# Optimization experiments

Hardware: AMD Instinct MI355X
Metric: run time of the kernel (lower is better)

Reference implementation:

```python
import jax, jax.numpy as jnp
import numpy as np

# static config (mirrors init_kwargs)
F_T, S = 8, 24            # video_shape = (F_T, S, S)
K, DIL = 3, 1             # kernel_size, dilation (same for all 3 axes)
HEADS, DHEAD, DIM = 8, 64, 512
INNER = HEADS * DHEAD
PAD = DIL * (K - 1)       # causal: pad 2 at the FRONT of each spatial axis
KJ = K ** 3               # 27 neighbors per query
N_VID = F_T * S * S       # 4608 video tokens


def causal_pad(t):
    # t: [B, D, F, S, S] -> pad front of f/h/w axes (torch F.pad (PAD*?,0) causal layout)
    return jnp.pad(t, ((0, 0), (0, 0), (PAD, 0), (PAD, 0), (PAD, 0)))


def unfold3d(t):
    # torch unfoldNd equivalent. t: [B, D, F+PAD, S+PAD, S+PAD]
    # returns [B, N_VID, KJ, D]; kernel offsets ordered (kf, kh, kw) w fastest,
    # matching torch unfold's channel-major / kernel-minor layout after the
    # rearrange 'b (d j) i -> b i j d'.
    sl = []
    for i in range(K):
        for j in range(K):
            for kk in range(K):
                sl.append(t[:, :, i * DIL:i * DIL + F_T,
                                  j * DIL:j * DIL + S,
                                  kk * DIL:kk * DIL + S])
    u = jnp.stack(sl, axis=2)                      # [B, D, KJ, F, S, S]
    B, D = t.shape[0], t.shape[1]
    u = u.reshape(B, D, KJ, N_VID)
    return jnp.transpose(u, (0, 3, 2, 1))          # [B, N_VID, KJ, D]


def make_mask():
    # True where the neighbor falls into zero padding (out-of-range / future under causal pad)
    ones = jnp.ones((1, 1, F_T, S, S), jnp.float32)
    u = unfold3d(causal_pad(ones))[0, :, :, 0]     # [N_VID, KJ]
    m = u == 0.0
    return jnp.pad(m, ((0, 0), (1, 0)), constant_values=False)  # bos col never masked


def stable_softmax(t, alpha=32.0 ** 2):
    t = t / alpha
    t = t - jax.lax.stop_gradient(jnp.max(t, axis=-1, keepdims=True))
    return jax.nn.softmax(t * alpha, axis=-1)


def setup_inputs() -> dict:
    key = jax.random.key(0)
    ks = jax.random.split(key, 9)
    return {
        "x": jax.random.normal(ks[0], (1, N_VID + 1, DIM), jnp.float32),
        "Wq": jax.random.normal(ks[1], (DIM, INNER), jnp.float32) * 0.02,
        "Wkv": jax.random.normal(ks[2], (DIM, 2 * INNER), jnp.float32) * 0.02,
        "W_th": jax.random.normal(ks[3], (HEADS, HEADS), jnp.float32) * 0.2,
        "Wout": jax.random.normal(ks[4], (INNER, DIM), jnp.float32) * 0.02,
        "bout": jax.random.normal(ks[5], (DIM,), jnp.float32) * 0.02,
        "ax1": jax.random.normal(ks[6], (K, HEADS), jnp.float32),
        "ax2": jax.random.normal(ks[7], (K, HEADS), jnp.float32),
        "ax3": jax.random.normal(ks[8], (K, HEADS), jnp.float32),
    }


def reference(x, Wq, Wkv, W_th, Wout, bout, ax1, ax2, ax3):
    b, n, _ = x.shape                       # b=1, n = 1 + N_VID (no extra padding)
    h, d = HEADS, DHEAD
    scale = d ** -0.5

    q = x @ Wq
    k, v = jnp.split(x @ Wkv, 2, axis=-1)

    def to_heads(t):  # 'b n (h d) -> (b h) n d'
        return t.reshape(b, n, h, d).transpose(0, 2, 1, 3).reshape(b * h, n, d)

    q, k, v = map(to_heads, (q, k, v))
    q = q[:, 1:] * scale                    # drop bos query
    k_bos, v_bos = k[:, :1], v[:, :1]       # [bh, 1, d]
    k, v = k[:, 1:], v[:, 1:]

    def to_vid(t):  # 'b (f h w) d -> b d f h w'
        return t.reshape(b * h, F_T, S, S, d).transpose(0, 4, 1, 2, 3)

    ku = unfold3d(causal_pad(to_vid(k)))    # [bh, N, KJ, d]
    vu = unfold3d(causal_pad(to_vid(v)))
    N = ku.shape[1]

    kb = jnp.broadcast_to(k_bos[:, :, None, :], (b * h, N, 1, d))
    vb = jnp.broadcast_to(v_bos[:, :, None, :], (b * h, N, 1, d))
    ku = jnp.concatenate([kb, ku], axis=2)  # [bh, N, KJ+1, d]
    vu = jnp.concatenate([vb, vu], axis=2)

    sim = jnp.einsum('bid,bijd->bij', q, ku)                 # [bh, N, KJ+1]

    # axial relative position bias over the 3x3x3 kernel, pad 0 for bos column
    rel = (ax1[:, None, None, :] + ax2[None, :, None, :] + ax3[None, None, :, :])
    rel = rel.reshape(KJ, h)                                 # [27, h]
    bias = jnp.pad(rel.T[:, None, :], ((0, 0), (0, 0), (1, 0)))  # [h, 1, KJ+1]

    sim = sim.reshape(b, h, N, KJ + 1) + bias[None]
    mask = make_mask()                                       # [N, KJ+1]
    sim = jnp.where(mask[None, None], -jnp.finfo(sim.dtype).max, sim)

    attn = stable_softmax(sim)                               # [b, h, N, KJ+1]
    attn = jnp.einsum('hg,bgij->bhij', W_th, attn)           # talking heads 1x1 conv

    out = jnp.einsum('bhij,bhijd->bhid', attn, vu.reshape(b, h, N, KJ + 1, d))
    out = jnp.concatenate([v_bos.reshape(b, h, 1, d), out], axis=2)  # re-attach bos value
    out = out.transpose(0, 2, 1, 3).reshape(b, n, h * d)     # '(b h) n d -> b n (h d)'
    return out @ Wout + bout
```

## Files before the change

### kernel.cpp

```cpp
#include <hip/hip_runtime.h>
#include <hip/hip_bf16.h>


constexpr int TFR   = 8;
constexpr int SDIM  = 24;
constexpr int NVID  = TFR * SDIM * SDIM;
constexpr int NTOK  = NVID + 1;
constexpr int NH    = 8;
constexpr int DM    = 512;
constexpr int NJ    = 28;

typedef __attribute__((ext_vector_type(8))) short bf16x8;
typedef __attribute__((ext_vector_type(8))) unsigned short ushort8;
typedef __attribute__((ext_vector_type(4))) float f32x4;

__device__ __forceinline__ float bf2f(unsigned short u) {
    return __uint_as_float((unsigned)u << 16);
}
__device__ __forceinline__ unsigned short f2bf(float f) {
    __hip_bfloat16 h = __float2bfloat16(f);
    return reinterpret_cast<unsigned short&>(h);
}

constexpr int CAST_BLOCKS = (NTOK * DM / 4 + 255) / 256;

__global__ __launch_bounds__(256)
void prep_kernel(const float* __restrict__ x,
                 const float* __restrict__ Wq, const float* __restrict__ Wkv,
                 const float* __restrict__ Wout,
                 __hip_bfloat16* __restrict__ Xb,
                 __hip_bfloat16* __restrict__ Wqkvt,
                 __hip_bfloat16* __restrict__ Woutt)
{
    const int b   = blockIdx.x;
    const int tid = threadIdx.x;

    if (b < CAST_BLOCKS) {
        const int i = (b * 256 + tid) * 4;
        if (i >= NTOK * DM) return;
        const float4 v = *(const float4*)(x + i);
        Xb[i + 0] = __float2bfloat16(v.x);
        Xb[i + 1] = __float2bfloat16(v.y);
        Xb[i + 2] = __float2bfloat16(v.z);
        Xb[i + 3] = __float2bfloat16(v.w);
        return;
    }

    __shared__ float t[32][33];
    int tb = b - CAST_BLOCKS;
    const float* W; __hip_bfloat16* Wt; int Nd, tX, rowOff;
    if (tb < 256)      { W = Wq;   Wt = Wqkvt; Nd = 512;  tX = 16; rowOff = 0;   }
    else if (tb < 768) { tb -= 256; W = Wkv;  Wt = Wqkvt; Nd = 1024; tX = 32; rowOff = 512; }
    else               { tb -= 768; W = Wout; Wt = Woutt; Nd = 512;  tX = 16; rowOff = 0;   }
    const int n0 = (tb % tX) * 32, k0 = (tb / tX) * 32;
    const int r  = tid >> 3;
    const int c4 = (tid & 7) * 4;
    const float4 v = *(const float4*)(W + (size_t)(k0 + r) * Nd + n0 + c4);
    t[r][c4 + 0] = v.x; t[r][c4 + 1] = v.y; t[r][c4 + 2] = v.z; t[r][c4 + 3] = v.w;
    __syncthreads();
    #pragma unroll
    for (int j = 0; j < 4; ++j)
        Wt[(size_t)(rowOff + n0 + r) * 512 + k0 + c4 + j] = __float2bfloat16(t[c4 + j][r]);
}

template<int MODE>
__global__ __launch_bounds__(256)
void gemm_bt(const __hip_bfloat16* __restrict__ A,
             const __hip_bfloat16* __restrict__ Bt,
             float* __restrict__ C, __hip_bfloat16* __restrict__ Cb,
             int M, int N, int K, const float* __restrict__ bias)
{
    constexpr int BM = 64, BN = 64, BK = 64, PITCH = 72;
    __shared__ short As[BM * PITCH];
    __shared__ short Bs[BN * PITCH];

    const int tid  = threadIdx.x;
    const int m0   = blockIdx.x * BM;
    const int n0   = blockIdx.y * BN;
    const int lane = tid & 63;
    const int wave = tid >> 6;
    const int wm   = (wave >> 1) * 32;
    const int wn   = (wave & 1) * 32;
    const int col  = lane & 15;
    const int quad = lane >> 4;

    f32x4 acc[2][2] = {};

    for (int k0 = 0; k0 < K; k0 += BK) {
        #pragma unroll
        for (int it = 0; it < 2; ++it) {
            const int idx = tid + it * 256;
            const int r = idx >> 3, c = idx & 7;
            const int gr = m0 + r;
            int4 val = make_int4(0, 0, 0, 0);
            if (gr < M)
                val = *(const int4*)(A + (size_t)gr * K + k0 + c * 8);
            *(int4*)(&As[r * PITCH + c * 8]) = val;
        }
        #pragma unroll
        for (int it = 0; it < 2; ++it) {
            const int idx = tid + it * 256;
            const int r = idx >> 3, c = idx & 7;
            const int4 val = *(const int4*)(Bt + (size_t)(n0 + r) * K + k0 + c * 8);
            *(int4*)(&Bs[r * PITCH + c * 8]) = val;
        }
        __syncthreads();

        #pragma unroll
        for (int ks = 0; ks < 2; ++ks) {
            bf16x8 af[2], bfr[2];
            #pragma unroll
            for (int mt = 0; mt < 2; ++mt)
                af[mt] = *(const bf16x8*)(&As[(wm + mt * 16 + col) * PITCH + ks * 32 + quad * 8]);
            #pragma unroll
            for (int nt = 0; nt < 2; ++nt)
                bfr[nt] = *(const bf16x8*)(&Bs[(wn + nt * 16 + col) * PITCH + ks * 32 + quad * 8]);
            #pragma unroll
            for (int mt = 0; mt < 2; ++mt)
                #pragma unroll
                for (int nt = 0; nt < 2; ++nt)
                    acc[mt][nt] = __builtin_amdgcn_mfma_f32_16x16x32_bf16(
                        af[mt], bfr[nt], acc[mt][nt], 0, 0, 0);
        }
        __syncthreads();
    }

    #pragma unroll
    for (int mt = 0; mt < 2; ++mt) {
        #pragma unroll
        for (int r = 0; r < 4; ++r) {
            const int row = m0 + wm + mt * 16 + quad * 4 + r;
            if (row >= M) continue;
            #pragma unroll
            for (int nt = 0; nt < 2; ++nt) {
                const int cg = n0 + wn + nt * 16 + col;
                float v = acc[mt][nt][r];
                if (MODE == 0) {
                    if (bias) v += bias[cg];
                    C[(size_t)row * N + cg] = v;
                } else {
                    if (cg < 512) C[(size_t)row * 512 + cg] = v;
                    else          Cb[(size_t)row * 1024 + (cg - 512)] = __float2bfloat16(v);
                }
            }
        }
    }
}

__global__ __launch_bounds__(256)
void attn_v2(const float* __restrict__ Q, const __hip_bfloat16* __restrict__ KVb,
             __hip_bfloat16* __restrict__ O,
             const float* __restrict__ W_th,
             const float* __restrict__ ax1, const float* __restrict__ ax2,
             const float* __restrict__ ax3)
{
    __shared__ float attn_s[4][NH * NJ];
    __shared__ float mixed_s[4][NH * NJ];

    const int tid  = threadIdx.x;
    const int wave = tid >> 6;
    const int lane = tid & 63;
    const int g    = lane >> 3;
    const int s    = lane & 7;
    const int i    = __builtin_amdgcn_readfirstlane(blockIdx.x * 4 + (tid >> 6));
    const int qrow = i + 1;

    const int t  = i / (SDIM * SDIM);
    const int rm = i % (SDIM * SDIM);
    const int y  = rm / SDIM;
    const int x  = rm % SDIM;

    float qf[8];
    {
        const float4 q0 = *(const float4*)(Q + (size_t)qrow * DM + lane * 8);
        const float4 q1 = *(const float4*)(Q + (size_t)qrow * DM + lane * 8 + 4);
        qf[0] = q0.x * 0.125f; qf[1] = q0.y * 0.125f; qf[2] = q0.z * 0.125f; qf[3] = q0.w * 0.125f;
        qf[4] = q1.x * 0.125f; qf[5] = q1.y * 0.125f; qf[6] = q1.z * 0.125f; qf[7] = q1.w * 0.125f;
    }
    float a1[3], a2[3], a3[3];
    #pragma unroll
    for (int d = 0; d < 3; ++d) {
        a1[d] = ax1[d * NH + g];
        a2[d] = ax2[d * NH + g];
        a3[d] = ax3[d * NH + g];
    }

    float sim[NJ];
    #pragma unroll
    for (int j = 0; j < NJ; ++j) {
        int row; bool valid; float bias;
        if (j == 0) { row = 0; valid = true; bias = 0.f; }
        else {
            const int jp = j - 1;
            const int di = jp / 9, dj = (jp / 3) % 3, dk = jp % 3;
            const int tt = t + di - 2, yy = y + dj - 2, xx = x + dk - 2;
            valid = (tt >= 0) && (yy >= 0) && (xx >= 0);
            row = 1 + tt * SDIM * SDIM + yy * SDIM + xx;
            bias = a1[di] + a2[dj] + a3[dk];
        }
        if (valid) {
            const ushort8 kv = *(const ushort8*)(KVb + (size_t)row * 1024 + lane * 8);
            float p = 0.f;
            #pragma unroll
            for (int e = 0; e < 8; ++e) p += bf2f(kv[e]) * qf[e];
            p += __shfl_xor(p, 1);
            p += __shfl_xor(p, 2);
            p += __shfl_xor(p, 4);
            sim[j] = p + bias;
        } else {
            sim[j] = -1e30f;
        }
    }

    float m = -1e30f;
    #pragma unroll
    for (int j = 0; j < NJ; ++j) m = fmaxf(m, sim[j]);
    float ssum = 0.f;
    #pragma unroll
    for (int j = 0; j < NJ; ++j) { sim[j] = __expf(sim[j] - m); ssum += sim[j]; }
    const float inv = 1.f / ssum;
    #pragma unroll
    for (int j = 0; j < NJ; ++j) sim[j] *= inv;

    if (s == 0) {
        #pragma unroll
        for (int u = 0; u < 7; ++u) {
            f32x4 v4 = { sim[4*u], sim[4*u+1], sim[4*u+2], sim[4*u+3] };
            *(f32x4*)(&attn_s[wave][g * NJ + 4 * u]) = v4;
        }
    }
    __syncthreads();

    if (tid < NH * NJ) {
        const int h = tid / NJ, j = tid % NJ;
        #pragma unroll
        for (int q = 0; q < 4; ++q) {
            float acc = 0.f;
            #pragma unroll
            for (int gg = 0; gg < NH; ++gg)
                acc += W_th[h * NH + gg] * attn_s[q][gg * NJ + j];
            mixed_s[q][h * NJ + j] = acc;
        }
    }
    __syncthreads();

    float acc8[8] = {};
    #pragma unroll
    for (int j = 0; j < NJ; ++j) {
        int row; bool valid;
        if (j == 0) { row = 0; valid = true; }
        else {
            const int jp = j - 1;
            const int di = jp / 9, dj = (jp / 3) % 3, dk = jp % 3;
            const int tt = t + di - 2, yy = y + dj - 2, xx = x + dk - 2;
            valid = (tt >= 0) && (yy >= 0) && (xx >= 0);
            row = 1 + tt * SDIM * SDIM + yy * SDIM + xx;
        }
        if (valid) {
            const ushort8 vv = *(const ushort8*)(KVb + (size_t)row * 1024 + 512 + lane * 8);
            const float w = mixed_s[wave][g * NJ + j];
            #pragma unroll
            for (int e = 0; e < 8; ++e) acc8[e] += w * bf2f(vv[e]);
        }
    }

    ushort8 o;
    #pragma unroll
    for (int e = 0; e < 8; ++e) o[e] = f2bf(acc8[e]);
    *(ushort8*)(O + (size_t)qrow * DM + lane * 8) = o;

    if (i == 0) {
        const ushort8 vb = *(const ushort8*)(KVb + 512 + lane * 8);
        *(ushort8*)(O + lane * 8) = vb;
    }
}

extern "C" void kernel_launch(void* const* d_in, const int* in_sizes, int n_in,
                              void* d_out, int out_size, void* d_ws, size_t ws_size,
                              hipStream_t stream)
{
    const float* x    = (const float*)d_in[0];
    const float* Wq   = (const float*)d_in[1];
    const float* Wkv  = (const float*)d_in[2];
    const float* W_th = (const float*)d_in[3];
    const float* Wout = (const float*)d_in[4];
    const float* bout = (const float*)d_in[5];
    const float* ax1  = (const float*)d_in[6];
    const float* ax2  = (const float*)d_in[7];
    const float* ax3  = (const float*)d_in[8];
    float* out = (float*)d_out;

    char* p = (char*)d_ws;
    float* Qf = (float*)p;                         p += (size_t)NTOK * DM * 4;
    __hip_bfloat16* KVb   = (__hip_bfloat16*)p;    p += (size_t)NTOK * 2 * DM * 2;
    __hip_bfloat16* Xb    = (__hip_bfloat16*)p;    p += (size_t)NTOK * DM * 2;
    __hip_bfloat16* Ob    = (__hip_bfloat16*)p;    p += (size_t)NTOK * DM * 2;
    __hip_bfloat16* Wqkvt = (__hip_bfloat16*)p;    p += (size_t)3 * DM * DM * 2;
    __hip_bfloat16* Woutt = (__hip_bfloat16*)p;    p += (size_t)DM * DM * 2;

    const dim3 blk(256);
    const int mtiles = (NTOK + 63) / 64;

    prep_kernel<<<CAST_BLOCKS + 1024, blk, 0, stream>>>(x, Wq, Wkv, Wout, Xb, Wqkvt, Woutt);

    gemm_bt<1><<<dim3(mtiles, 24), blk, 0, stream>>>(Xb, Wqkvt, Qf, KVb,
                                                     NTOK, 3 * DM, DM, nullptr);

    attn_v2<<<dim3(NVID / 4), blk, 0, stream>>>(Qf, KVb, Ob, W_th, ax1, ax2, ax3);

    gemm_bt<0><<<dim3(mtiles, 8), blk, 0, stream>>>(Ob, Woutt, out, nullptr,
                                                    NTOK, DM, DM, bout);
}
```

Baseline: 141.6 us.

## Enlarge GEMM tiles and load tiles directly into XOR-swizzled LDS

Replaces the fixed 64x64 GEMM with a templated MFMA GEMM using 128x128 tiles for the QKV projection and 128x64 tiles for the output projection. Each wave now computes up to 4x4 MFMA tiles. Tiles are loaded with global_load_lds straight into LDS, using an XOR swizzle instead of padded rows to avoid bank conflicts. The aim is more data reuse per block and fewer register round-trips on loads. In exchange it drops the row bounds guard, so the last M tile reads past the input into adjacent workspace; those rows are discarded.

```diff
diff --git a/kernel.cpp b/kernel.cpp
--- a/kernel.cpp
+++ b/kernel.cpp
@@ -14,12 +14,11 @@
 typedef __attribute__((ext_vector_type(8))) unsigned short ushort8;
 typedef __attribute__((ext_vector_type(4))) float f32x4;
 
+typedef const __attribute__((address_space(1))) unsigned int* gas_ptr;
+typedef __attribute__((address_space(3))) unsigned int* las_ptr;
+
 __device__ __forceinline__ float bf2f(unsigned short u) {
     return __uint_as_float((unsigned)u << 16);
-}
-__device__ __forceinline__ unsigned short f2bf(float f) {
-    __hip_bfloat16 h = __float2bfloat16(f);
-    return reinterpret_cast<unsigned short&>(h);
 }
 
 constexpr int CAST_BLOCKS = (NTOK * DM / 4 + 255) / 256;
@@ -63,84 +62,93 @@
         Wt[(size_t)(rowOff + n0 + r) * 512 + k0 + c4 + j] = __float2bfloat16(t[c4 + j][r]);
 }
 
-template<int MODE>
+template<int BM, int BN, int AM, int AN, int MODE>
 __global__ __launch_bounds__(256)
-void gemm_bt(const __hip_bfloat16* __restrict__ A,
-             const __hip_bfloat16* __restrict__ Bt,
-             float* __restrict__ C, __hip_bfloat16* __restrict__ Cb,
-             int M, int N, int K, const float* __restrict__ bias)
+void gemm_mfma(const __hip_bfloat16* __restrict__ A,
+               const __hip_bfloat16* __restrict__ Bt,
+               float* __restrict__ C, __hip_bfloat16* __restrict__ Cb,
+               int M, int N, int K, const float* __restrict__ bias)
 {
-    constexpr int BM = 64, BN = 64, BK = 64, PITCH = 72;
-    __shared__ short As[BM * PITCH];
-    __shared__ short Bs[BN * PITCH];
+    constexpr int BK = 64;
+    __shared__ __align__(16) short As[BM * BK];
+    __shared__ __align__(16) short Bs[BN * BK];
 
     const int tid  = threadIdx.x;
     const int m0   = blockIdx.x * BM;
     const int n0   = blockIdx.y * BN;
     const int lane = tid & 63;
     const int wave = tid >> 6;
-    const int wm   = (wave >> 1) * 32;
-    const int wn   = (wave & 1) * 32;
+    const int wm   = (wave >> 1) * (AM * 16);
+    const int wn   = (wave & 1) * (AN * 16);
     const int col  = lane & 15;
     const int quad = lane >> 4;
 
-    f32x4 acc[2][2] = {};
+    f32x4 acc[AM][AN] = {};
 
     for (int k0 = 0; k0 < K; k0 += BK) {
         #pragma unroll
-        for (int it = 0; it < 2; ++it) {
-            const int idx = tid + it * 256;
-            const int r = idx >> 3, c = idx & 7;
-            const int gr = m0 + r;
-            int4 val = make_int4(0, 0, 0, 0);
-            if (gr < M)
-                val = *(const int4*)(A + (size_t)gr * K + k0 + c * 8);
-            *(int4*)(&As[r * PITCH + c * 8]) = val;
-        }
-        #pragma unroll
-        for (int it = 0; it < 2; ++it) {
-            const int idx = tid + it * 256;
-            const int r = idx >> 3, c = idx & 7;
-            const int4 val = *(const int4*)(Bt + (size_t)(n0 + r) * K + k0 + c * 8);
-            *(int4*)(&Bs[r * PITCH + c * 8]) = val;
+        for (int it = 0; it < BM * 8 / 256; ++it) {
+            const int idx = it * 256 + tid;
+            const int r   = idx >> 3;
+            const int u   = (idx & 7) ^ (r & 7);
+            const __hip_bfloat16* gp = A + (size_t)(m0 + r) * K + k0 + u * 8;
+            __builtin_amdgcn_global_load_lds(
+                (gas_ptr)gp, (las_ptr)&As[(it * 256 + wave * 64) * 8], 16, 0, 0);
+        }
+        #pragma unroll
+        for (int it = 0; it < BN * 8 / 256; ++it) {
+            const int idx = it * 256 + tid;
+            const int r   = idx >> 3;
+            const int u   = (idx & 7) ^ (r & 7);
+            const __hip_bfloat16* gp = Bt + (size_t)(n0 + r) * K + k0 + u * 8;
+            __builtin_amdgcn_global_load_lds(
+                (gas_ptr)gp, (las_ptr)&Bs[(it * 256 + wave * 64) * 8], 16, 0, 0);
         }
         __syncthreads();
 
         #pragma unroll
         for (int ks = 0; ks < 2; ++ks) {
-            bf16x8 af[2], bfr[2];
-            #pragma unroll
-            for (int mt = 0; mt < 2; ++mt)
-                af[mt] = *(const bf16x8*)(&As[(wm + mt * 16 + col) * PITCH + ks * 32 + quad * 8]);
-            #pragma unroll
-            for (int nt = 0; nt < 2; ++nt)
-                bfr[nt] = *(const bf16x8*)(&Bs[(wn + nt * 16 + col) * PITCH + ks * 32 + quad * 8]);
-            #pragma unroll
-            for (int mt = 0; mt < 2; ++mt)
+            bf16x8 af[AM], bfr[AN];
+            #pragma unroll
+            for (int mt = 0; mt < AM; ++mt) {
+                const int r = wm + mt * 16 + col;
+                const int u = (ks * 4 + quad) ^ (r & 7);
+                af[mt] = *(const bf16x8*)(&As[r * BK + u * 8]);
+            }
+            #pragma unroll
+            for (int nt = 0; nt < AN; ++nt) {
+                const int r = wn + nt * 16 + col;
+                const int u = (ks * 4 + quad) ^ (r & 7);
+                bfr[nt] = *(const bf16x8*)(&Bs[r * BK + u * 8]);
+            }
+            #pragma unroll
+            for (int mt = 0; mt < AM; ++mt)
                 #pragma unroll
-                for (int nt = 0; nt < 2; ++nt)
+                for (int nt = 0; nt < AN; ++nt)
                     acc[mt][nt] = __builtin_amdgcn_mfma_f32_16x16x32_bf16(
                         af[mt], bfr[nt], acc[mt][nt], 0, 0, 0);
         }
         __syncthreads();
     }
 
-    #pragma unroll
-    for (int mt = 0; mt < 2; ++mt) {
+    const bool isQ = (MODE == 1) && (n0 < 512);
+    #pragma unroll
+    for (int mt = 0; mt < AM; ++mt) {
         #pragma unroll
         for (int r = 0; r < 4; ++r) {
             const int row = m0 + wm + mt * 16 + quad * 4 + r;
             if (row >= M) continue;
             #pragma unroll
-            for (int nt = 0; nt < 2; ++nt) {
+            for (int nt = 0; nt < AN; ++nt) {
                 const int cg = n0 + wn + nt * 16 + col;
                 float v = acc[mt][nt][r];
                 if (MODE == 0) {
                     if (bias) v += bias[cg];
                     C[(size_t)row * N + cg] = v;
+                } else if (isQ) {
+                    C[(size_t)row * 512 + cg] = v;
                 } else {
-                    if (cg < 512) C[(size_t)row * 512 + cg] = v;
-                    else          Cb[(size_t)row * 1024 + (cg - 512)] = __float2bfloat16(v);
+                    Cb[(size_t)row * 1024 + (cg - 512)] = __float2bfloat16(v);
                 }
             }
         }
@@ -264,10 +272,10 @@
         }
     }
 
-    ushort8 o;
-    #pragma unroll
-    for (int e = 0; e < 8; ++e) o[e] = f2bf(acc8[e]);
-    *(ushort8*)(O + (size_t)qrow * DM + lane * 8) = o;
+    __hip_bfloat16 o[8];
+    #pragma unroll
+    for (int e = 0; e < 8; ++e) o[e] = __float2bfloat16(acc8[e]);
+    *(ushort8*)(O + (size_t)qrow * DM + lane * 8) = *(const ushort8*)o;
 
     if (i == 0) {
         const ushort8 vb = *(const ushort8*)(KVb + 512 + lane * 8);
@@ -299,15 +307,15 @@
     __hip_bfloat16* Woutt = (__hip_bfloat16*)p;    p += (size_t)DM * DM * 2;
 
     const dim3 blk(256);
-    const int mtiles = (NTOK + 63) / 64;
+    const int mtiles = (NTOK + 127) / 128;
 
     prep_kernel<<<CAST_BLOCKS + 1024, blk, 0, stream>>>(x, Wq, Wkv, Wout, Xb, Wqkvt, Woutt);
 
-    gemm_bt<1><<<dim3(mtiles, 24), blk, 0, stream>>>(Xb, Wqkvt, Qf, KVb,
-                                                     NTOK, 3 * DM, DM, nullptr);
+    gemm_mfma<128, 128, 4, 4, 1><<<dim3(mtiles, 12), blk, 0, stream>>>(
+        Xb, Wqkvt, Qf, KVb, NTOK, 3 * DM, DM, nullptr);
 
     attn_v2<<<dim3(NVID / 4), blk, 0, stream>>>(Qf, KVb, Ob, W_th, ax1, ax2, ax3);
 
-    gemm_bt<0><<<dim3(mtiles, 8), blk, 0, stream>>>(Ob, Woutt, out, nullptr,
-                                                    NTOK, DM, DM, bout);
-}
+    gemm_mfma<128, 64, 4, 2, 0><<<dim3(mtiles, 8), blk, 0, stream>>>(
+        Ob, Woutt, out, nullptr, NTOK, DM, DM, bout);
+}
```

After: 140.2 us. No clear change (-1.0%).

## Fuse fp32-to-bf16 casts into GEMM loads and enlarge GEMM tiles

Applied to the files above, without the earlier changes.

Drops the separate prep kernel that cast x and transposed the weights to bf16. Both GEMMs now read fp32 A and untransposed fp32 B directly and convert to bf16 while staging into shared memory. Tiles grow from 64x64 to 128x128, the Q 1/8 scale moves into the GEMM epilogue, and the attention output becomes fp32. This saves a launch and the bf16 intermediates, but doubles global read bytes for the operands, adds transpose-scatter stores to LDS, and cuts the grid to far fewer blocks (37x12 and 37x4), which may underfill the GPU.

```diff
diff --git a/kernel.cpp b/kernel.cpp
--- a/kernel.cpp
+++ b/kernel.cpp
@@ -22,55 +22,15 @@
     return reinterpret_cast<unsigned short&>(h);
 }
 
-constexpr int CAST_BLOCKS = (NTOK * DM / 4 + 255) / 256;
-
-__global__ __launch_bounds__(256)
-void prep_kernel(const float* __restrict__ x,
-                 const float* __restrict__ Wq, const float* __restrict__ Wkv,
-                 const float* __restrict__ Wout,
-                 __hip_bfloat16* __restrict__ Xb,
-                 __hip_bfloat16* __restrict__ Wqkvt,
-                 __hip_bfloat16* __restrict__ Woutt)
-{
-    const int b   = blockIdx.x;
-    const int tid = threadIdx.x;
-
-    if (b < CAST_BLOCKS) {
-        const int i = (b * 256 + tid) * 4;
-        if (i >= NTOK * DM) return;
-        const float4 v = *(const float4*)(x + i);
-        Xb[i + 0] = __float2bfloat16(v.x);
-        Xb[i + 1] = __float2bfloat16(v.y);
-        Xb[i + 2] = __float2bfloat16(v.z);
-        Xb[i + 3] = __float2bfloat16(v.w);
-        return;
-    }
-
-    __shared__ float t[32][33];
-    int tb = b - CAST_BLOCKS;
-    const float* W; __hip_bfloat16* Wt; int Nd, tX, rowOff;
-    if (tb < 256)      { W = Wq;   Wt = Wqkvt; Nd = 512;  tX = 16; rowOff = 0;   }
-    else if (tb < 768) { tb -= 256; W = Wkv;  Wt = Wqkvt; Nd = 1024; tX = 32; rowOff = 512; }
-    else               { tb -= 768; W = Wout; Wt = Woutt; Nd = 512;  tX = 16; rowOff = 0;   }
-    const int n0 = (tb % tX) * 32, k0 = (tb / tX) * 32;
-    const int r  = tid >> 3;
-    const int c4 = (tid & 7) * 4;
-    const float4 v = *(const float4*)(W + (size_t)(k0 + r) * Nd + n0 + c4);
-    t[r][c4 + 0] = v.x; t[r][c4 + 1] = v.y; t[r][c4 + 2] = v.z; t[r][c4 + 3] = v.w;
-    __syncthreads();
-    #pragma unroll
-    for (int j = 0; j < 4; ++j)
-        Wt[(size_t)(rowOff + n0 + r) * 512 + k0 + c4 + j] = __float2bfloat16(t[c4 + j][r]);
-}
-
 template<int MODE>
 __global__ __launch_bounds__(256)
-void gemm_bt(const __hip_bfloat16* __restrict__ A,
-             const __hip_bfloat16* __restrict__ Bt,
-             float* __restrict__ C, __hip_bfloat16* __restrict__ Cb,
-             int M, int N, int K, const float* __restrict__ bias)
+void gemm_f32src(const float* __restrict__ A,
+                 const float* __restrict__ B1,
+                 const float* __restrict__ B2,
+                 float* __restrict__ C, __hip_bfloat16* __restrict__ Cb,
+                 int M, int N, const float* __restrict__ bias)
 {
-    constexpr int BM = 64, BN = 64, BK = 64, PITCH = 72;
+    constexpr int BM = 128, BN = 128, BK = 64, PITCH = 72, K = 512;
     __shared__ short As[BM * PITCH];
     __shared__ short Bs[BN * PITCH];
 
@@ -79,68 +39,82 @@
     const int n0   = blockIdx.y * BN;
     const int lane = tid & 63;
     const int wave = tid >> 6;
-    const int wm   = (wave >> 1) * 32;
-    const int wn   = (wave & 1) * 32;
+    const int wm   = (wave >> 1) * 64;
+    const int wn   = (wave & 1) * 64;
     const int col  = lane & 15;
     const int quad = lane >> 4;
 
-    f32x4 acc[2][2] = {};
+    const float* Bsrc; int bpitch, col0;
+    if (MODE == 1 && n0 >= 512) { Bsrc = B2; bpitch = 1024; col0 = n0 - 512; }
+    else                        { Bsrc = B1; bpitch = 512;  col0 = n0; }
+
+    f32x4 acc[4][4] = {};
 
     for (int k0 = 0; k0 < K; k0 += BK) {
         #pragma unroll
-        for (int it = 0; it < 2; ++it) {
-            const int idx = tid + it * 256;
-            const int r = idx >> 3, c = idx & 7;
-            const int gr = m0 + r;
-            int4 val = make_int4(0, 0, 0, 0);
-            if (gr < M)
-                val = *(const int4*)(A + (size_t)gr * K + k0 + c * 8);
-            *(int4*)(&As[r * PITCH + c * 8]) = val;
-        }
-        #pragma unroll
-        for (int it = 0; it < 2; ++it) {
-            const int idx = tid + it * 256;
-            const int r = idx >> 3, c = idx & 7;
-            const int4 val = *(const int4*)(Bt + (size_t)(n0 + r) * K + k0 + c * 8);
-            *(int4*)(&Bs[r * PITCH + c * 8]) = val;
+        for (int r = 0; r < 4; ++r) {
+            const int m  = (tid >> 3) + r * 32;
+            const int k8 = (tid & 7) * 8;
+            const int gm = (m0 + m < M) ? (m0 + m) : (M - 1);
+            const float4 f0 = *(const float4*)(A + (size_t)gm * K + k0 + k8);
+            const float4 f1 = *(const float4*)(A + (size_t)gm * K + k0 + k8 + 4);
+            unsigned short v[8] = { f2bf(f0.x), f2bf(f0.y), f2bf(f0.z), f2bf(f0.w),
+                                    f2bf(f1.x), f2bf(f1.y), f2bf(f1.z), f2bf(f1.w) };
+            *(ushort8*)(&As[m * PITCH + k8]) = *(const ushort8*)v;
+        }
+        #pragma unroll
+        for (int r = 0; r < 4; ++r) {
+            const int p = (tid >> 4) + (r >> 1) * 16;
+            const int n = (tid & 15) * 4 + (r & 1) * 64;
+            const float4 f0 = *(const float4*)(Bsrc + (size_t)(k0 + 2 * p)     * bpitch + col0 + n);
+            const float4 f1 = *(const float4*)(Bsrc + (size_t)(k0 + 2 * p + 1) * bpitch + col0 + n);
+            const float e0[4] = { f0.x, f0.y, f0.z, f0.w };
+            const float e1[4] = { f1.x, f1.y, f1.z, f1.w };
+            #pragma unroll
+            for (int e = 0; e < 4; ++e) {
+                const unsigned pk = (unsigned)f2bf(e0[e]) | ((unsigned)f2bf(e1[e]) << 16);
+                *(unsigned*)(&Bs[(n + e) * PITCH + 2 * p]) = pk;
+            }
         }
         __syncthreads();
 
         #pragma unroll
         for (int ks = 0; ks < 2; ++ks) {
-            bf16x8 af[2], bfr[2];
-            #pragma unroll
-            for (int mt = 0; mt < 2; ++mt)
+            bf16x8 af[4], bfr[4];
+            #pragma unroll
+            for (int mt = 0; mt < 4; ++mt)
                 af[mt] = *(const bf16x8*)(&As[(wm + mt * 16 + col) * PITCH + ks * 32 + quad * 8]);
             #pragma unroll
-            for (int nt = 0; nt < 2; ++nt)
+            for (int nt = 0; nt < 4; ++nt)
                 bfr[nt] = *(const bf16x8*)(&Bs[(wn + nt * 16 + col) * PITCH + ks * 32 + quad * 8]);
             #pragma unroll
-            for (int mt = 0; mt < 2; ++mt)
+            for (int mt = 0; mt < 4; ++mt)
                 #pragma unroll
-                for (int nt = 0; nt < 2; ++nt)
+                for (int nt = 0; nt < 4; ++nt)
                     acc[mt][nt] = __builtin_amdgcn_mfma_f32_16x16x32_bf16(
                         af[mt], bfr[nt], acc[mt][nt], 0, 0, 0);
         }
         __syncthreads();
     }
 
-    #pragma unroll
-    for (int mt = 0; mt < 2; ++mt) {
+    const bool isQ = (MODE == 1) && (n0 < 512);
+    #pragma unroll
+    for (int mt = 0; mt < 4; ++mt) {
         #pragma unroll
         for (int r = 0; r < 4; ++r) {
             const int row = m0 + wm + mt * 16 + quad * 4 + r;
             if (row >= M) continue;
             #pragma unroll
-            for (int nt = 0; nt < 2; ++nt) {
+            for (int nt = 0; nt < 4; ++nt) {
                 const int cg = n0 + wn + nt * 16 + col;
                 float v = acc[mt][nt][r];
                 if (MODE == 0) {
                     if (bias) v += bias[cg];
                     C[(size_t)row * N + cg] = v;
+                } else if (isQ) {
+                    C[(size_t)row * 512 + cg] = v * 0.125f;
                 } else {
-                    if (cg < 512) C[(size_t)row * 512 + cg] = v;
-                    else          Cb[(size_t)row * 1024 + (cg - 512)] = __float2bfloat16(v);
+                    Cb[(size_t)row * 1024 + (cg - 512)] = __float2bfloat16(v);
                 }
             }
         }
@@ -149,7 +123,7 @@
 
 __global__ __launch_bounds__(256)
 void attn_v2(const float* __restrict__ Q, const __hip_bfloat16* __restrict__ KVb,
-             __hip_bfloat16* __restrict__ O,
+             float* __restrict__ O,
              const float* __restrict__ W_th,
              const float* __restrict__ ax1, const float* __restrict__ ax2,
              const float* __restrict__ ax3)
@@ -174,8 +148,8 @@
     {
         const float4 q0 = *(const float4*)(Q + (size_t)qrow * DM + lane * 8);
         const float4 q1 = *(const float4*)(Q + (size_t)qrow * DM + lane * 8 + 4);
-        qf[0] = q0.x * 0.125f; qf[1] = q0.y * 0.125f; qf[2] = q0.z * 0.125f; qf[3] = q0.w * 0.125f;
-        qf[4] = q1.x * 0.125f; qf[5] = q1.y * 0.125f; qf[6] = q1.z * 0.125f; qf[7] = q1.w * 0.125f;
+        qf[0] = q0.x; qf[1] = q0.y; qf[2] = q0.z; qf[3] = q0.w;
+        qf[4] = q1.x; qf[5] = q1.y; qf[6] = q1.z; qf[7] = q1.w;
     }
     float a1[3], a2[3], a3[3];
     #pragma unroll
@@ -264,14 +238,17 @@
         }
     }
 
-    ushort8 o;
-    #pragma unroll
-    for (int e = 0; e < 8; ++e) o[e] = f2bf(acc8[e]);
-    *(ushort8*)(O + (size_t)qrow * DM + lane * 8) = o;
+    float4 o0 = { acc8[0], acc8[1], acc8[2], acc8[3] };
+    float4 o1 = { acc8[4], acc8[5], acc8[6], acc8[7] };
+    *(float4*)(O + (size_t)qrow * DM + lane * 8)     = o0;
+    *(float4*)(O + (size_t)qrow * DM + lane * 8 + 4) = o1;
 
     if (i == 0) {
         const ushort8 vb = *(const ushort8*)(KVb + 512 + lane * 8);
-        *(ushort8*)(O + lane * 8) = vb;
+        float4 b0 = { bf2f(vb[0]), bf2f(vb[1]), bf2f(vb[2]), bf2f(vb[3]) };
+        float4 b1 = { bf2f(vb[4]), bf2f(vb[5]), bf2f(vb[6]), bf2f(vb[7]) };
+        *(float4*)(O + lane * 8)     = b0;
+        *(float4*)(O + lane * 8 + 4) = b1;
     }
 }
 
@@ -291,23 +268,18 @@
     float* out = (float*)d_out;
 
     char* p = (char*)d_ws;
-    float* Qf = (float*)p;                         p += (size_t)NTOK * DM * 4;
-    __hip_bfloat16* KVb   = (__hip_bfloat16*)p;    p += (size_t)NTOK * 2 * DM * 2;
-    __hip_bfloat16* Xb    = (__hip_bfloat16*)p;    p += (size_t)NTOK * DM * 2;
-    __hip_bfloat16* Ob    = (__hip_bfloat16*)p;    p += (size_t)NTOK * DM * 2;
-    __hip_bfloat16* Wqkvt = (__hip_bfloat16*)p;    p += (size_t)3 * DM * DM * 2;
-    __hip_bfloat16* Woutt = (__hip_bfloat16*)p;    p += (size_t)DM * DM * 2;
+    float* Qf = (float*)p;                       p += (size_t)NTOK * DM * 4;
+    __hip_bfloat16* KVb = (__hip_bfloat16*)p;    p += (size_t)NTOK * 2 * DM * 2;
+    float* Of = (float*)p;                       p += (size_t)NTOK * DM * 4;
 
     const dim3 blk(256);
-    const int mtiles = (NTOK + 63) / 64;
-
-    prep_kernel<<<CAST_BLOCKS + 1024, blk, 0, stream>>>(x, Wq, Wkv, Wout, Xb, Wqkvt, Woutt);
-
-    gemm_bt<1><<<dim3(mtiles, 24), blk, 0, stream>>>(Xb, Wqkvt, Qf, KVb,
-                                                     NTOK, 3 * DM, DM, nullptr);
-
-    attn_v2<<<dim3(NVID / 4), blk, 0, stream>>>(Qf, KVb, Ob, W_th, ax1, ax2, ax3);
-
-    gemm_bt<0><<<dim3(mtiles, 8), blk, 0, stream>>>(Ob, Woutt, out, nullptr,
-                                                    NTOK, DM, DM, bout);
-}
+    const int mtiles = (NTOK + 127) / 128;
+
+    gemm_f32src<1><<<dim3(mtiles, 12), blk, 0, stream>>>(
+        x, Wq, Wkv, Qf, KVb, NTOK, 3 * DM, nullptr);
+
+    attn_v2<<<dim3(NVID / 4), blk, 0, stream>>>(Qf, KVb, Of, W_th, ax1, ax2, ax3);
+
+    gemm_f32src<0><<<dim3(mtiles, 4), blk, 0, stream>>>(
+        Of, Wout, nullptr, out, nullptr, NTOK, DM, bout);
+}
```

Measured after the change: 156.8 us. 1.11x slower.
